# Kernel optimization log

Measured on AMD Instinct MI355X. Metric: run time of the kernel, lower is better.

Reference implementation:

```python
import jax, jax.numpy as jnp
import numpy as np
from jax.scipy.linalg import expm

B = 1048576
M = 6
N = 3
VAR = 1.0


def setup_inputs() -> dict:
    key = jax.random.key(0)
    k1, k2, k3 = jax.random.split(key, 3)
    x = jax.random.normal(k1, (B, N, 1), dtype=jnp.float32)
    c = jax.random.normal(k2, (B, M), dtype=jnp.float32)
    # psi init: randn * (var / N), per stable_init=False branch
    psi = jax.random.normal(k3, (M, N, N), dtype=jnp.float32) * (VAR / N)
    return {"x": x, "c": c, "psi": psi}


def reference(x, c, psi):
    # T[b] = sum_m c[b,m] * psi[m]  -> [B, N, N]
    T = jnp.einsum('bm,mpk->bpk', c, psi)
    # batched small-matrix exponential (scaling-and-squaring Pade, as torch.matrix_exp)
    expT = jax.vmap(expm)(T)  # [B, N, N]
    # apply transported operator to points x: [B, N, 1]
    return expT @ x
```

## Files before the change

kernel.cpp:

```cpp
#include <hip/hip_runtime.h>
#include <math.h>

constexpr int MM = 6;

__device__ __forceinline__ void mm3(const float A[9], const float B[9], float C[9]) {
#pragma unroll
    for (int i = 0; i < 3; ++i) {
#pragma unroll
        for (int j = 0; j < 3; ++j) {
            C[i * 3 + j] = fmaf(A[i * 3 + 0], B[0 * 3 + j],
                           fmaf(A[i * 3 + 1], B[1 * 3 + j],
                                A[i * 3 + 2] * B[2 * 3 + j]));
        }
    }
}

__global__ __launch_bounds__(256) void expm_apply4_kernel(
    const float4* __restrict__ x4,
    const float4* __restrict__ c4,
    const float* __restrict__ psi,
    float4* __restrict__ out4,
    int nthread)
{
    __shared__ float spsi[MM * 9];
    if (threadIdx.x < MM * 9) spsi[threadIdx.x] = psi[threadIdx.x];
    __syncthreads();

    int t = blockIdx.x * blockDim.x + threadIdx.x;
    if (t >= nthread) return;

    float4 q0 = c4[(size_t)t * 6 + 0];
    float4 q1 = c4[(size_t)t * 6 + 1];
    float4 q2 = c4[(size_t)t * 6 + 2];
    float4 q3 = c4[(size_t)t * 6 + 3];
    float4 q4 = c4[(size_t)t * 6 + 4];
    float4 q5 = c4[(size_t)t * 6 + 5];
    float cm[4][MM] = {
        {q0.x, q0.y, q0.z, q0.w, q1.x, q1.y},
        {q1.z, q1.w, q2.x, q2.y, q2.z, q2.w},
        {q3.x, q3.y, q3.z, q3.w, q4.x, q4.y},
        {q4.z, q4.w, q5.x, q5.y, q5.z, q5.w}};

    float4 r0 = x4[(size_t)t * 3 + 0];
    float4 r1 = x4[(size_t)t * 3 + 1];
    float4 r2 = x4[(size_t)t * 3 + 2];
    float xx[4][3] = {{r0.x, r0.y, r0.z},
                      {r0.w, r1.x, r1.y},
                      {r1.z, r1.w, r2.x},
                      {r2.y, r2.z, r2.w}};

    float T[4][9];
#pragma unroll
    for (int i = 0; i < 9; ++i) {
        float p0 = spsi[i];
#pragma unroll
        for (int e = 0; e < 4; ++e) T[e][i] = cm[e][0] * p0;
#pragma unroll
        for (int m = 1; m < MM; ++m) {
            float p = spsi[m * 9 + i];
#pragma unroll
            for (int e = 0; e < 4; ++e) T[e][i] = fmaf(cm[e][m], p, T[e][i]);
        }
    }

    float y[4][3];
#pragma unroll
    for (int e = 0; e < 4; ++e) {
        float ra = fabsf(T[e][0]) + fabsf(T[e][1]) + fabsf(T[e][2]);
        float rb = fabsf(T[e][3]) + fabsf(T[e][4]) + fabsf(T[e][5]);
        float rc = fabsf(T[e][6]) + fabsf(T[e][7]) + fabsf(T[e][8]);
        float a = fmaxf(ra, fmaxf(rb, rc));

        int ex;
        (void)frexpf(a * (1.0f / 1.8f), &ex);
        int s = min(max(ex, 0), 4);
        float sc = ldexpf(1.0f, -s);

        float A[9];
#pragma unroll
        for (int i = 0; i < 9; ++i) A[i] = T[e][i] * sc;

        float A2[9], A4[9];
        mm3(A, A, A2);
        mm3(A2, A2, A4);

        float P[9], U[9], V[9];
#pragma unroll
        for (int i = 0; i < 9; ++i) P[i] = fmaf(420.f, A2[i], A4[i]);
        P[0] += 15120.f; P[4] += 15120.f; P[8] += 15120.f;
        mm3(A, P, U);
#pragma unroll
        for (int i = 0; i < 9; ++i) V[i] = fmaf(30.f, A4[i], 3360.f * A2[i]);
        V[0] += 30240.f; V[4] += 30240.f; V[8] += 30240.f;

        float Mn[9], R[9];
#pragma unroll
        for (int i = 0; i < 9; ++i) { Mn[i] = V[i] - U[i]; R[i] = V[i] + U[i]; }

        float inv[9];
        inv[0] = Mn[4] * Mn[8] - Mn[5] * Mn[7];
        inv[1] = Mn[2] * Mn[7] - Mn[1] * Mn[8];
        inv[2] = Mn[1] * Mn[5] - Mn[2] * Mn[4];
        inv[3] = Mn[5] * Mn[6] - Mn[3] * Mn[8];
        inv[4] = Mn[0] * Mn[8] - Mn[2] * Mn[6];
        inv[5] = Mn[2] * Mn[3] - Mn[0] * Mn[5];
        inv[6] = Mn[3] * Mn[7] - Mn[4] * Mn[6];
        inv[7] = Mn[1] * Mn[6] - Mn[0] * Mn[7];
        inv[8] = Mn[0] * Mn[4] - Mn[1] * Mn[3];
        float det = Mn[0] * inv[0] + Mn[1] * inv[3] + Mn[2] * inv[6];
        float rdet = 1.0f / det;

        float X[9];
        mm3(inv, R, X);
#pragma unroll
        for (int i = 0; i < 9; ++i) X[i] *= rdet;

        for (int it = 0; it < 4; ++it) {
            if (!__any(it < s)) break;
            float t2[9];
            mm3(X, X, t2);
            bool doit = it < s;
#pragma unroll
            for (int i = 0; i < 9; ++i) X[i] = doit ? t2[i] : X[i];
        }

        y[e][0] = fmaf(X[0], xx[e][0], fmaf(X[1], xx[e][1], X[2] * xx[e][2]));
        y[e][1] = fmaf(X[3], xx[e][0], fmaf(X[4], xx[e][1], X[5] * xx[e][2]));
        y[e][2] = fmaf(X[6], xx[e][0], fmaf(X[7], xx[e][1], X[8] * xx[e][2]));
    }

    out4[(size_t)t * 3 + 0] = make_float4(y[0][0], y[0][1], y[0][2], y[1][0]);
    out4[(size_t)t * 3 + 1] = make_float4(y[1][1], y[1][2], y[2][0], y[2][1]);
    out4[(size_t)t * 3 + 2] = make_float4(y[2][2], y[3][0], y[3][1], y[3][2]);
}

extern "C" void kernel_launch(void* const* d_in, const int* in_sizes, int n_in,
                              void* d_out, int out_size, void* d_ws, size_t ws_size,
                              hipStream_t stream) {
    const float4* x4   = (const float4*)d_in[0];
    const float4* c4   = (const float4*)d_in[1];
    const float* psi   = (const float*)d_in[2];
    float4* out4 = (float4*)d_out;
    int B = in_sizes[0] / 3;
    int nthread = B / 4;

    int block = 256;
    int grid = (nthread + block - 1) / block;
    expm_apply4_kernel<<<grid, block, 0, stream>>>(x4, c4, psi, out4, nthread);
}
```

Before: 18.54 us.

## Process two items per thread and replace final squarings with vector reapplication

Each thread now handles two batch elements instead of four, which doubles the thread count, and psi is read straight into registers instead of being staged through shared memory with a barrier. The scaling exponent is floored at 2. Only the squarings beyond two are done as 3x3 matrix products; the remaining factor of four is applied by multiplying the 3-vector by X four times, replacing two matrix squarings with four mat-vec products. This trims arithmetic and divergence, but it always scales by at least 4, which changes rounding slightly, and the smaller vector loads and stores may reduce memory efficiency.

```diff
diff --git a/kernel.cpp b/kernel.cpp
--- a/kernel.cpp
+++ b/kernel.cpp
@@ -15,70 +15,56 @@
     }
 }
 
-__global__ __launch_bounds__(256) void expm_apply4_kernel(
-    const float4* __restrict__ x4,
+__global__ __launch_bounds__(256) void expm_apply2_kernel(
+    const float2* __restrict__ x2,
     const float4* __restrict__ c4,
     const float* __restrict__ psi,
-    float4* __restrict__ out4,
+    float2* __restrict__ out2,
     int nthread)
 {
-    __shared__ float spsi[MM * 9];
-    if (threadIdx.x < MM * 9) spsi[threadIdx.x] = psi[threadIdx.x];
-    __syncthreads();
-
     int t = blockIdx.x * blockDim.x + threadIdx.x;
     if (t >= nthread) return;
 
-    float4 q0 = c4[(size_t)t * 6 + 0];
-    float4 q1 = c4[(size_t)t * 6 + 1];
-    float4 q2 = c4[(size_t)t * 6 + 2];
-    float4 q3 = c4[(size_t)t * 6 + 3];
-    float4 q4 = c4[(size_t)t * 6 + 4];
-    float4 q5 = c4[(size_t)t * 6 + 5];
-    float cm[4][MM] = {
-        {q0.x, q0.y, q0.z, q0.w, q1.x, q1.y},
-        {q1.z, q1.w, q2.x, q2.y, q2.z, q2.w},
-        {q3.x, q3.y, q3.z, q3.w, q4.x, q4.y},
-        {q4.z, q4.w, q5.x, q5.y, q5.z, q5.w}};
+    float sp[54];
+#pragma unroll
+    for (int i = 0; i < 54; ++i) sp[i] = psi[i];
 
-    float4 r0 = x4[(size_t)t * 3 + 0];
-    float4 r1 = x4[(size_t)t * 3 + 1];
-    float4 r2 = x4[(size_t)t * 3 + 2];
-    float xx[4][3] = {{r0.x, r0.y, r0.z},
-                      {r0.w, r1.x, r1.y},
-                      {r1.z, r1.w, r2.x},
-                      {r2.y, r2.z, r2.w}};
+    float4 q0 = c4[(size_t)t * 3 + 0];
+    float4 q1 = c4[(size_t)t * 3 + 1];
+    float4 q2 = c4[(size_t)t * 3 + 2];
+    float cm[2][MM] = {{q0.x, q0.y, q0.z, q0.w, q1.x, q1.y},
+                       {q1.z, q1.w, q2.x, q2.y, q2.z, q2.w}};
 
-    float T[4][9];
+    float2 r0 = x2[(size_t)t * 3 + 0];
+    float2 r1 = x2[(size_t)t * 3 + 1];
+    float2 r2 = x2[(size_t)t * 3 + 2];
+    float xx[2][3] = {{r0.x, r0.y, r1.x}, {r1.y, r2.x, r2.y}};
+
+    float y[2][3];
 #pragma unroll
-    for (int i = 0; i < 9; ++i) {
-        float p0 = spsi[i];
+    for (int e = 0; e < 2; ++e) {
+        float T[9];
 #pragma unroll
-        for (int e = 0; e < 4; ++e) T[e][i] = cm[e][0] * p0;
+        for (int i = 0; i < 9; ++i) {
+            float acc = cm[e][0] * sp[i];
 #pragma unroll
-        for (int m = 1; m < MM; ++m) {
-            float p = spsi[m * 9 + i];
-#pragma unroll
-            for (int e = 0; e < 4; ++e) T[e][i] = fmaf(cm[e][m], p, T[e][i]);
+            for (int m = 1; m < MM; ++m) acc = fmaf(cm[e][m], sp[m * 9 + i], acc);
+            T[i] = acc;
         }
-    }
 
-    float y[4][3];
-#pragma unroll
-    for (int e = 0; e < 4; ++e) {
-        float ra = fabsf(T[e][0]) + fabsf(T[e][1]) + fabsf(T[e][2]);
-        float rb = fabsf(T[e][3]) + fabsf(T[e][4]) + fabsf(T[e][5]);
-        float rc = fabsf(T[e][6]) + fabsf(T[e][7]) + fabsf(T[e][8]);
+        float ra = fabsf(T[0]) + fabsf(T[1]) + fabsf(T[2]);
+        float rb = fabsf(T[3]) + fabsf(T[4]) + fabsf(T[5]);
+        float rc = fabsf(T[6]) + fabsf(T[7]) + fabsf(T[8]);
         float a = fmaxf(ra, fmaxf(rb, rc));
 
         int ex;
         (void)frexpf(a * (1.0f / 1.8f), &ex);
-        int s = min(max(ex, 0), 4);
+        int s = min(max(ex, 2), 4);
         float sc = ldexpf(1.0f, -s);
 
         float A[9];
 #pragma unroll
-        for (int i = 0; i < 9; ++i) A[i] = T[e][i] * sc;
+        for (int i = 0; i < 9; ++i) A[i] = T[i] * sc;
 
         float A2[9], A4[9];
         mm3(A, A, A2);
@@ -115,36 +101,42 @@
 #pragma unroll
         for (int i = 0; i < 9; ++i) X[i] *= rdet;
 
-        for (int it = 0; it < 4; ++it) {
-            if (!__any(it < s)) break;
+        for (int it = 0; it < 2; ++it) {
+            if (!__any(it < s - 2)) break;
             float t2[9];
             mm3(X, X, t2);
-            bool doit = it < s;
+            bool d = it < s - 2;
 #pragma unroll
-            for (int i = 0; i < 9; ++i) X[i] = doit ? t2[i] : X[i];
+            for (int i = 0; i < 9; ++i) X[i] = d ? t2[i] : X[i];
         }
 
-        y[e][0] = fmaf(X[0], xx[e][0], fmaf(X[1], xx[e][1], X[2] * xx[e][2]));
-        y[e][1] = fmaf(X[3], xx[e][0], fmaf(X[4], xx[e][1], X[5] * xx[e][2]));
-        y[e][2] = fmaf(X[6], xx[e][0], fmaf(X[7], xx[e][1], X[8] * xx[e][2]));
+        float v0 = xx[e][0], v1 = xx[e][1], v2 = xx[e][2];
+#pragma unroll
+        for (int k = 0; k < 4; ++k) {
+            float w0 = fmaf(X[0], v0, fmaf(X[1], v1, X[2] * v2));
+            float w1 = fmaf(X[3], v0, fmaf(X[4], v1, X[5] * v2));
+            float w2 = fmaf(X[6], v0, fmaf(X[7], v1, X[8] * v2));
+            v0 = w0; v1 = w1; v2 = w2;
+        }
+        y[e][0] = v0; y[e][1] = v1; y[e][2] = v2;
     }
 
-    out4[(size_t)t * 3 + 0] = make_float4(y[0][0], y[0][1], y[0][2], y[1][0]);
-    out4[(size_t)t * 3 + 1] = make_float4(y[1][1], y[1][2], y[2][0], y[2][1]);
-    out4[(size_t)t * 3 + 2] = make_float4(y[2][2], y[3][0], y[3][1], y[3][2]);
+    out2[(size_t)t * 3 + 0] = make_float2(y[0][0], y[0][1]);
+    out2[(size_t)t * 3 + 1] = make_float2(y[0][2], y[1][0]);
+    out2[(size_t)t * 3 + 2] = make_float2(y[1][1], y[1][2]);
 }
 
 extern "C" void kernel_launch(void* const* d_in, const int* in_sizes, int n_in,
                               void* d_out, int out_size, void* d_ws, size_t ws_size,
                               hipStream_t stream) {
-    const float4* x4   = (const float4*)d_in[0];
+    const float2* x2   = (const float2*)d_in[0];
     const float4* c4   = (const float4*)d_in[1];
     const float* psi   = (const float*)d_in[2];
-    float4* out4 = (float4*)d_out;
+    float2* out2 = (float2*)d_out;
     int B = in_sizes[0] / 3;
-    int nthread = B / 4;
+    int nthread = B / 2;
 
     int block = 256;
     int grid = (nthread + block - 1) / block;
-    expm_apply4_kernel<<<grid, block, 0, stream>>>(x4, c4, psi, out4, nthread);
+    expm_apply2_kernel<<<grid, block, 0, stream>>>(x2, c4, psi, out2, nthread);
 }
```

Result: faster. 16.80 us (-9.4%).
